# Optimization experiments

Hardware: AMD Instinct MI355X
Metric: run time of the kernel (lower is better)

## Reference

```python
import jax, jax.numpy as jnp
import numpy as np

E4M3_MAX = 448.0  # max representable value of float8_e4m3fn


def _updated_scale(amax_history, amax_now, scale):
    # roll history, insert current amax, take running max (delayed scaling)
    hist = jnp.roll(amax_history, 1).at[0].set(amax_now)
    amax = jnp.max(hist)
    sf = E4M3_MAX / amax  # scale factor (margin = 0)
    sf = jnp.where((amax > 0.0) & jnp.isfinite(amax), sf, 1.0 / scale)
    return 1.0 / sf  # dequant scale


def _qdq(x, scale, amax_history):
    # quantize-dequantize through float8_e4m3fn with dynamic amax-history scaling
    amax_now = jnp.max(jnp.abs(x)).astype(jnp.float32)
    s = _updated_scale(amax_history, amax_now, scale[0])
    q = jnp.clip(x / s, -E4M3_MAX, E4M3_MAX).astype(jnp.float8_e4m3fn)
    return q.astype(x.dtype) * s


def setup_inputs() -> dict:
    key = jax.random.key(0)
    k1, k2 = jax.random.split(key, 2)
    B, S, D, F = 4, 2048, 4096, 16384
    HL = 16  # amax_history_length
    inputs = jax.random.normal(k1, (B, S, D), jnp.float32)
    # lecun_normal: std = 1/sqrt(fan_in)
    kernel = jax.random.normal(k2, (D, F), jnp.float32) * (1.0 / np.sqrt(D))
    bias = jnp.zeros((F,), jnp.float32)
    return {
        "inputs": inputs,
        "kernel": kernel,
        "bias": bias,
        "input_scale": jnp.ones((1,), jnp.float32),
        "input_amax_history": jnp.zeros((HL,), jnp.float32),
        "kernel_scale": jnp.ones((1,), jnp.float32),
        "kernel_amax_history": jnp.zeros((HL,), jnp.float32),
        "output_grad_scale": jnp.ones((1,), jnp.float32),
        "output_grad_amax_history": jnp.zeros((HL,), jnp.float32),
    }


def reference(inputs, kernel, bias, input_scale, input_amax_history,
              kernel_scale, kernel_amax_history, output_grad_scale,
              output_grad_amax_history):
    B, S, D = inputs.shape
    x = inputs.reshape(-1, D)  # (B*S, D)
    q_x = _qdq(x, input_scale, input_amax_history)
    q_k = _qdq(kernel, kernel_scale, kernel_amax_history)
    out = q_x @ q_k  # (B*S, F)
    # bias is rounded fp32->bf16->fp32 per the module
    b = bias.astype(jnp.bfloat16).astype(jnp.float32)
    out = jax.nn.gelu(out + b)
    return out.reshape(B, S, -1)
```

## Files before the change

kernel.cpp:

```cpp
#include <hip/hip_runtime.h>
#include <hip/hip_bf16.h>

typedef __attribute__((ext_vector_type(4))) int i32x4;
typedef __attribute__((ext_vector_type(8))) int i32x8;
typedef __attribute__((ext_vector_type(16))) float f32x16;

#define E4M3_MAX 448.0f
#define AS1 __attribute__((address_space(1)))
#define AS3 __attribute__((address_space(3)))

__device__ __forceinline__ float clip448(float v) {
  return fminf(fmaxf(v, -E4M3_MAX), E4M3_MAX);
}

__device__ __forceinline__ void gld_lds16(const void* g, void* l) {
  __builtin_amdgcn_global_load_lds((const AS1 void*)g, (AS3 void*)l, 16, 0, 0);
}

__device__ __forceinline__ float gelu_f(float v) {
  float y = 0.7978845608028654f * (v + 0.044715f * v * v * v);
  float a = fabsf(y);
  float z = __expf(-2.f * a);
  float th = (1.f - z) / (1.f + z);
  th = copysignf(th, y);
  return 0.5f * v * (1.f + th);
}

__global__ void init_ws_kernel(unsigned int* amax) {
  amax[0] = 0u;
  amax[1] = 0u;
}

__global__ void amax_kernel(const float* __restrict__ x, long n4,
                            unsigned int* __restrict__ amax_out) {
  long i0 = (long)blockIdx.x * blockDim.x + threadIdx.x;
  long stride = (long)gridDim.x * blockDim.x;
  const float4* x4 = (const float4*)x;
  float m = 0.f;
  for (long i = i0; i < n4; i += stride) {
    float4 v = x4[i];
    m = fmaxf(m, fmaxf(fmaxf(fabsf(v.x), fabsf(v.y)), fmaxf(fabsf(v.z), fabsf(v.w))));
  }
#pragma unroll
  for (int off = 32; off >= 1; off >>= 1)
    m = fmaxf(m, __shfl_xor(m, off));
  __shared__ float wmax[8];
  int wid = threadIdx.x >> 6;
  if ((threadIdx.x & 63) == 0) wmax[wid] = m;
  __syncthreads();
  if (threadIdx.x == 0) {
    int nw = blockDim.x >> 6;
    float bm = wmax[0];
    for (int w = 1; w < nw; ++w) bm = fmaxf(bm, wmax[w]);
    atomicMax(amax_out, __float_as_uint(bm));
  }
}

__global__ void scale_kernel(const unsigned int* __restrict__ amax,
                             const float* __restrict__ scale_x,
                             const float* __restrict__ hist_x,
                             const float* __restrict__ scale_k,
                             const float* __restrict__ hist_k,
                             int hl, float* __restrict__ scales) {
  if (threadIdx.x != 0) return;
  float ax = __uint_as_float(amax[0]);
  for (int i = 0; i < hl - 1; ++i) ax = fmaxf(ax, hist_x[i]);
  float sfx = E4M3_MAX / ax;
  if (!(ax > 0.f && isfinite(ax))) sfx = 1.f / scale_x[0];
  float sx = 1.f / sfx;
  float ak = __uint_as_float(amax[1]);
  for (int i = 0; i < hl - 1; ++i) ak = fmaxf(ak, hist_k[i]);
  float sfk = E4M3_MAX / ak;
  if (!(ak > 0.f && isfinite(ak))) sfk = 1.f / scale_k[0];
  float sk = 1.f / sfk;
  scales[0] = sx;
  scales[1] = sk;
  scales[2] = sx * sk;
}


__global__ void quant_x_kernel(const float* __restrict__ x,
                               unsigned char* __restrict__ Aq,
                               const float* __restrict__ scales, int K) {
  const float s = scales[0];
  const int kt = blockIdx.x, mt = blockIdx.y, nkt = gridDim.x;
  __shared__ float lt[128][68];
  const int t = threadIdx.x;
  const float* src = x + (size_t)mt * 128 * K + (size_t)kt * 64;
#pragma unroll
  for (int it = 0; it < 8; ++it) {
    int row = it * 16 + (t >> 4);
    int c4 = (t & 15) * 4;
    float4 v = *(const float4*)&src[(size_t)row * K + c4];
    lt[row][c4 + 0] = v.x; lt[row][c4 + 1] = v.y;
    lt[row][c4 + 2] = v.z; lt[row][c4 + 3] = v.w;
  }
  __syncthreads();
  uint4* out = (uint4*)(Aq + ((size_t)mt * nkt + kt) * 8192);
#pragma unroll
  for (int cc = 0; cc < 2; ++cc) {
    int c = t * 2 + cc;
    int g = c >> 7, h = (c >> 6) & 1, l = c & 63;
    int row = g * 32 + (l & 31);
    int kb = (l >> 5) * 32 + h * 16;
    unsigned int w[4];
#pragma unroll
    for (int q = 0; q < 4; ++q) {
      int b = kb + q * 4;
      int p = 0;
      p = __builtin_amdgcn_cvt_pk_fp8_f32(clip448(lt[row][b+0] / s), clip448(lt[row][b+1] / s), p, false);
      p = __builtin_amdgcn_cvt_pk_fp8_f32(clip448(lt[row][b+2] / s), clip448(lt[row][b+3] / s), p, true);
      w[q] = (unsigned int)p;
    }
    out[c] = make_uint4(w[0], w[1], w[2], w[3]);
  }
}

__global__ void quant_k_kernel(const float* __restrict__ w,
                               unsigned char* __restrict__ Bq,
                               const float* __restrict__ scales, int N) {
  const float s = scales[1];
  const int kt = blockIdx.x, nt = blockIdx.y, nkt = gridDim.x;
  __shared__ float lt[64][132];
  const int t = threadIdx.x;
  const float* src = w + (size_t)kt * 64 * N + (size_t)nt * 128;
#pragma unroll
  for (int it = 0; it < 8; ++it) {
    int row = it * 8 + (t >> 5);
    int c4 = (t & 31) * 4;
    float4 v = *(const float4*)&src[(size_t)row * N + c4];
    lt[row][c4 + 0] = v.x; lt[row][c4 + 1] = v.y;
    lt[row][c4 + 2] = v.z; lt[row][c4 + 3] = v.w;
  }
  __syncthreads();
  uint4* out = (uint4*)(Bq + ((size_t)nt * nkt + kt) * 8192);
#pragma unroll
  for (int cc = 0; cc < 2; ++cc) {
    int c = t * 2 + cc;
    int g = c >> 7, h = (c >> 6) & 1, l = c & 63;
    int nl = g * 32 + (l & 31);
    int kb = (l >> 5) * 32 + h * 16;
    unsigned int w4[4];
#pragma unroll
    for (int q = 0; q < 4; ++q) {
      int b = kb + q * 4;
      int p = 0;
      p = __builtin_amdgcn_cvt_pk_fp8_f32(clip448(lt[b+0][nl] / s), clip448(lt[b+1][nl] / s), p, false);
      p = __builtin_amdgcn_cvt_pk_fp8_f32(clip448(lt[b+2][nl] / s), clip448(lt[b+3][nl] / s), p, true);
      w4[q] = (unsigned int)p;
    }
    out[c] = make_uint4(w4[0], w4[1], w4[2], w4[3]);
  }
}

#define BUFSZ 32768

#define RD_AV(dst, g_)                                                         \
  {                                                                            \
    const unsigned char* p_ =                                                  \
        lds + cb + ((g_) >> 2) * 8192 + ((g_) & 3) * 2048 + lane * 16;         \
    i32x4 lo_ = *(const i32x4*)p_;                                             \
    i32x4 hi_ = *(const i32x4*)(p_ + 1024);                                    \
    dst = __builtin_shufflevector(lo_, hi_, 0, 1, 2, 3, 4, 5, 6, 7);           \
  }
#define RD_BV(dst, g_)                                                         \
  {                                                                            \
    const unsigned char* p_ =                                                  \
        lds + cb + 16384 + ((g_) >> 2) * 8192 + ((g_) & 3) * 2048 + lane * 16; \
    i32x4 lo_ = *(const i32x4*)p_;                                             \
    i32x4 hi_ = *(const i32x4*)(p_ + 1024);                                    \
    dst = __builtin_shufflevector(lo_, hi_, 0, 1, 2, 3, 4, 5, 6, 7);           \
  }
#define MFMA1(r_, c_, a_, b_)                                                  \
  acc[r_][c_] = __builtin_amdgcn_mfma_scale_f32_32x32x64_f8f6f4(               \
      a_, b_, acc[r_][c_], 0, 0, 0, 127, 0, 127);

__global__ __launch_bounds__(512, 2) void gemm_fp8_kernel(
    const unsigned char* __restrict__ Aq, const unsigned char* __restrict__ Bq,
    const float* __restrict__ bias, const float* __restrict__ scales,
    float* __restrict__ C, int M, int N, int K) {
  __shared__ __align__(16) unsigned char lds[4 * BUFSZ];
  const float s_xk = scales[2];
  const int nkt = K >> 6;
  const int t = threadIdx.x;
  const int lane = t & 63;
  const int wid = t >> 6;
  const int wm = wid >> 2, wn = wid & 3;

  int f = blockIdx.y * gridDim.x + blockIdx.x;
  int cpx = (gridDim.x * gridDim.y) >> 3;
  int f2 = (f & 7) * cpx + (f >> 3);
  int bx = f2 % gridDim.x;
  int by = f2 / gridDim.x;

  const size_t strideT = (size_t)nkt * 8192;
  const unsigned char* gA = Aq + (size_t)(2 * by) * strideT + t * 16;
  const unsigned char* gB = Bq + (size_t)(2 * bx) * strideT + t * 16;

  f32x16 acc[4][2];
#pragma unroll
  for (int i = 0; i < 4; ++i)
#pragma unroll
    for (int j = 0; j < 2; ++j)
#pragma unroll
      for (int r = 0; r < 16; ++r) acc[i][j][r] = 0.f;

  auto stage = [&](unsigned bufbase, int kt_) {
    size_t o = (size_t)kt_ * 8192;
    unsigned char* l = lds + bufbase + wid * 1024;
    gld_lds16(gA + o,           l);
    gld_lds16(gA + strideT + o, l + 8192);
    gld_lds16(gB + o,           l + 16384);
    gld_lds16(gB + strideT + o, l + 24576);
  };

  i32x8 av0, av1, av2, av3, bv0, bv1;

  stage(0 * BUFSZ, 0);
  stage(1 * BUFSZ, 1);

  for (int kt = 0; kt < nkt; ++kt) {
    const unsigned cb = (kt & 3) * BUFSZ;

    if (kt + 2 < nkt) {
      stage(((kt + 2) & 3) * BUFSZ, kt + 2);
      asm volatile("s_waitcnt vmcnt(8)" ::: "memory");
    } else if (kt + 1 < nkt) {
      asm volatile("s_waitcnt vmcnt(4)" ::: "memory");
    } else {
      asm volatile("s_waitcnt vmcnt(0)" ::: "memory");
    }
    __builtin_amdgcn_s_barrier();
    asm volatile("" ::: "memory");

    RD_AV(av0, wm * 4 + 0);
    RD_BV(bv0, wn * 2 + 0);
    RD_BV(bv1, wn * 2 + 1);
    RD_AV(av1, wm * 4 + 1);
    RD_AV(av2, wm * 4 + 2);
    RD_AV(av3, wm * 4 + 3);

    MFMA1(0, 0, av0, bv0); MFMA1(0, 1, av0, bv1);
    MFMA1(1, 0, av1, bv0); MFMA1(1, 1, av1, bv1);
    MFMA1(2, 0, av2, bv0); MFMA1(2, 1, av2, bv1);
    MFMA1(3, 0, av3, bv0); MFMA1(3, 1, av3, bv1);
  }

  const int m0 = by * 256;
  const int n0 = bx * 256;
  float bb[2];
#pragma unroll
  for (int j = 0; j < 2; ++j) {
    int col = n0 + wn * 64 + j * 32 + (lane & 31);
    bb[j] = __bfloat162float(__float2bfloat16(bias[col]));
  }
#pragma unroll
  for (int i = 0; i < 4; ++i) {
    int rowbase = m0 + wm * 128 + i * 32 + 4 * (lane >> 5);
#pragma unroll
    for (int j = 0; j < 2; ++j) {
      int col = n0 + wn * 64 + j * 32 + (lane & 31);
#pragma unroll
      for (int r = 0; r < 16; ++r) {
        int row = rowbase + (r & 3) + 8 * (r >> 2);
        float v = acc[i][j][r] * s_xk + bb[j];
        __builtin_nontemporal_store(gelu_f(v), &C[(size_t)row * N + col]);
      }
    }
  }
}

extern "C" void kernel_launch(void* const* d_in, const int* in_sizes, int n_in,
                              void* d_out, int out_size, void* d_ws, size_t ws_size,
                              hipStream_t stream) {
  const float* inputs = (const float*)d_in[0];
  const float* kernelw = (const float*)d_in[1];
  const float* bias = (const float*)d_in[2];
  const float* input_scale = (const float*)d_in[3];
  const float* input_hist = (const float*)d_in[4];
  const float* kernel_scale = (const float*)d_in[5];
  const float* kernel_hist = (const float*)d_in[6];

  const int F = in_sizes[2];
  const int D = in_sizes[1] / F;
  const long M = (long)in_sizes[0] / D;
  const int HL = in_sizes[4];
  const int N = F, K = D;

  unsigned int* amax = (unsigned int*)d_ws;
  float* scales = (float*)((char*)d_ws + 16);
  unsigned char* Aq = (unsigned char*)d_ws + 64;
  unsigned char* Bq = Aq + (size_t)M * K;

  float* C = (float*)d_out;

  init_ws_kernel<<<1, 1, 0, stream>>>(amax);
  amax_kernel<<<2048, 256, 0, stream>>>(inputs, (long)M * K / 4, &amax[0]);
  amax_kernel<<<2048, 256, 0, stream>>>(kernelw, (long)K * N / 4, &amax[1]);
  scale_kernel<<<1, 64, 0, stream>>>(amax, input_scale, input_hist, kernel_scale,
                                     kernel_hist, HL, scales);
  quant_x_kernel<<<dim3(K / 64, M / 128), 256, 0, stream>>>(inputs, Aq, scales, K);
  quant_k_kernel<<<dim3(K / 64, N / 128), 256, 0, stream>>>(kernelw, Bq, scales, N);
  gemm_fp8_kernel<<<dim3(N / 256, M / 256), 512, 0, stream>>>(Aq, Bq, bias, scales, C,
                                                              (int)M, N, K);
}
```

Baseline: 730.6 us.

## Load B fragments directly from global into registers, stage only A in LDS

Result: slower. 811.8 us (+11.1%).

```diff
diff --git a/kernel.cpp b/kernel.cpp
--- a/kernel.cpp
+++ b/kernel.cpp
@@ -153,7 +153,7 @@
   }
 }
 
-#define BUFSZ 32768
+#define BUFSZ 16384
 
 #define RD_AV(dst, g_)                                                         \
   {                                                                            \
@@ -163,17 +163,51 @@
     i32x4 hi_ = *(const i32x4*)(p_ + 1024);                                    \
     dst = __builtin_shufflevector(lo_, hi_, 0, 1, 2, 3, 4, 5, 6, 7);           \
   }
-#define RD_BV(dst, g_)                                                         \
+
+#define LOADB(pre, kt_)                                                        \
   {                                                                            \
-    const unsigned char* p_ =                                                  \
-        lds + cb + 16384 + ((g_) >> 2) * 8192 + ((g_) & 3) * 2048 + lane * 16; \
-    i32x4 lo_ = *(const i32x4*)p_;                                             \
-    i32x4 hi_ = *(const i32x4*)(p_ + 1024);                                    \
-    dst = __builtin_shufflevector(lo_, hi_, 0, 1, 2, 3, 4, 5, 6, 7);           \
-  }
+    const i32x4* p0_ = (const i32x4*)(gB0 + (size_t)(kt_) * 8192);             \
+    const i32x4* p1_ = (const i32x4*)(gB1 + (size_t)(kt_) * 8192);             \
+    pre##0 = p0_[0];                                                           \
+    pre##1 = p0_[64];                                 \
+    pre##2 = p1_[0];                                                           \
+    pre##3 = p1_[64];                                                          \
+  }
+
 #define MFMA1(r_, c_, a_, b_)                                                  \
   acc[r_][c_] = __builtin_amdgcn_mfma_scale_f32_32x32x64_f8f6f4(               \
       a_, b_, acc[r_][c_], 0, 0, 0, 127, 0, 127);
+
+#define TILE_SEG(curpre, nxtpre, kt_)                                          \
+  {                                                                            \
+    if ((kt_) + 1 < nkt) LOADB(nxtpre, (kt_) + 1);                             \
+    if ((kt_) + 2 < nkt) stageA((((kt_) + 2) & 3) * BUFSZ, (kt_) + 2);         \
+    if ((kt_) + 2 < nkt) {                                                     \
+      asm volatile("s_waitcnt vmcnt(8)" ::: "memory");                         \
+    } else if ((kt_) + 1 < nkt) {                                              \
+      asm volatile("s_waitcnt vmcnt(6)" ::: "memory");                         \
+    } else {                                                                   \
+      asm volatile("s_waitcnt vmcnt(0)" ::: "memory");                         \
+    }                                                                          \
+    __builtin_amdgcn_sched_barrier(0);                                         \
+    __builtin_amdgcn_s_barrier();                                              \
+    {                                                                          \
+      const unsigned cb = ((kt_) & 3) * BUFSZ;                                 \
+      i32x8 av0, av1, av2, av3;                                                \
+      RD_AV(av0, wm * 4 + 0);                                                  \
+      RD_AV(av1, wm * 4 + 1);                                                  \
+      RD_AV(av2, wm * 4 + 2);                                                  \
+      RD_AV(av3, wm * 4 + 3);                                                  \
+      i32x8 bv0 =                                                              \
+          __builtin_shufflevector(curpre##0, curpre##1, 0, 1, 2, 3, 4, 5, 6, 7); \
+      i32x8 bv1 =                                                              \
+          __builtin_shufflevector(curpre##2, curpre##3, 0, 1, 2, 3, 4, 5, 6, 7); \
+      MFMA1(0, 0, av0, bv0); MFMA1(0, 1, av0, bv1);                            \
+      MFMA1(1, 0, av1, bv0); MFMA1(1, 1, av1, bv1);                            \
+      MFMA1(2, 0, av2, bv0); MFMA1(2, 1, av2, bv1);                            \
+      MFMA1(3, 0, av3, bv0); MFMA1(3, 1, av3, bv1);                            \
+    }                                                                          \
+  }
 
 __global__ __launch_bounds__(512, 2) void gemm_fp8_kernel(
     const unsigned char* __restrict__ Aq, const unsigned char* __restrict__ Bq,
@@ -195,7 +229,12 @@
 
   const size_t strideT = (size_t)nkt * 8192;
   const unsigned char* gA = Aq + (size_t)(2 * by) * strideT + t * 16;
-  const unsigned char* gB = Bq + (size_t)(2 * bx) * strideT + t * 16;
+
+  const int g0 = wn * 2 + 0, g1 = wn * 2 + 1;
+  const unsigned char* gB0 =
+      Bq + (size_t)(2 * bx + (g0 >> 2)) * strideT + (g0 & 3) * 2048 + lane * 16;
+  const unsigned char* gB1 =
+      Bq + (size_t)(2 * bx + (g1 >> 2)) * strideT + (g1 & 3) * 2048 + lane * 16;
 
   f32x16 acc[4][2];
 #pragma unroll
@@ -205,45 +244,26 @@
 #pragma unroll
       for (int r = 0; r < 16; ++r) acc[i][j][r] = 0.f;
 
-  auto stage = [&](unsigned bufbase, int kt_) {
+  auto stageA = [&](unsigned bufbase, int kt_) {
     size_t o = (size_t)kt_ * 8192;
     unsigned char* l = lds + bufbase + wid * 1024;
     gld_lds16(gA + o,           l);
     gld_lds16(gA + strideT + o, l + 8192);
-    gld_lds16(gB + o,           l + 16384);
-    gld_lds16(gB + strideT + o, l + 24576);
   };
 
-  i32x8 av0, av1, av2, av3, bv0, bv1;
-
-  stage(0 * BUFSZ, 0);
-  stage(1 * BUFSZ, 1);
-
-  for (int kt = 0; kt < nkt; ++kt) {
-    const unsigned cb = (kt & 3) * BUFSZ;
-
-    if (kt + 2 < nkt) {
-      stage(((kt + 2) & 3) * BUFSZ, kt + 2);
-      asm volatile("s_waitcnt vmcnt(8)" ::: "memory");
-    } else if (kt + 1 < nkt) {
-      asm volatile("s_waitcnt vmcnt(4)" ::: "memory");
-    } else {
-      asm volatile("s_waitcnt vmcnt(0)" ::: "memory");
-    }
-    __builtin_amdgcn_s_barrier();
-    asm volatile("" ::: "memory");
-
-    RD_AV(av0, wm * 4 + 0);
-    RD_BV(bv0, wn * 2 + 0);
-    RD_BV(bv1, wn * 2 + 1);
-    RD_AV(av1, wm * 4 + 1);
-    RD_AV(av2, wm * 4 + 2);
-    RD_AV(av3, wm * 4 + 3);
-
-    MFMA1(0, 0, av0, bv0); MFMA1(0, 1, av0, bv1);
-    MFMA1(1, 0, av1, bv0); MFMA1(1, 1, av1, bv1);
-    MFMA1(2, 0, av2, bv0); MFMA1(2, 1, av2, bv1);
-    MFMA1(3, 0, av3, bv0); MFMA1(3, 1, av3, bv1);
+  i32x4 bAr0, bAr1, bAr2, bAr3;
+  i32x4 bBr0, bBr1, bBr2, bBr3;
+
+  stageA(0 * BUFSZ, 0);
+  stageA(1 * BUFSZ, 1);
+  LOADB(bAr, 0);
+  asm volatile("s_waitcnt vmcnt(0)" ::: "memory");
+  __builtin_amdgcn_sched_barrier(0);
+  __builtin_amdgcn_s_barrier();
+
+  for (int kt = 0; kt < nkt; kt += 2) {
+    TILE_SEG(bAr, bBr, kt);
+    TILE_SEG(bBr, bAr, kt + 1);
   }
 
   const int m0 = by * 256;
```

## Double-buffer LDS fragment registers to overlap reads with MFMA

Applied to the files above, without the earlier changes.

Result: slower. 1.386 ms (+89.7%).

```diff
diff --git a/kernel.cpp b/kernel.cpp
--- a/kernel.cpp
+++ b/kernel.cpp
@@ -155,25 +155,36 @@
 
 #define BUFSZ 32768
 
-#define RD_AV(dst, g_)                                                         \
+#define RD8(dst, byteoff)                                                      \
   {                                                                            \
-    const unsigned char* p_ =                                                  \
-        lds + cb + ((g_) >> 2) * 8192 + ((g_) & 3) * 2048 + lane * 16;         \
+    const unsigned char* p_ = lds + (byteoff) + lane * 16;                     \
     i32x4 lo_ = *(const i32x4*)p_;                                             \
     i32x4 hi_ = *(const i32x4*)(p_ + 1024);                                    \
     dst = __builtin_shufflevector(lo_, hi_, 0, 1, 2, 3, 4, 5, 6, 7);           \
   }
-#define RD_BV(dst, g_)                                                         \
+
+#define READ_FRAGS(pre, bufbase)                                               \
   {                                                                            \
-    const unsigned char* p_ =                                                  \
-        lds + cb + 16384 + ((g_) >> 2) * 8192 + ((g_) & 3) * 2048 + lane * 16; \
-    i32x4 lo_ = *(const i32x4*)p_;                                             \
-    i32x4 hi_ = *(const i32x4*)(p_ + 1024);                                    \
-    dst = __builtin_shufflevector(lo_, hi_, 0, 1, 2, 3, 4, 5, 6, 7);           \
-  }
+    const unsigned cb_ = (bufbase);                                            \
+    RD8(pre##a0, cb_ + ag0);                                                   \
+    RD8(pre##a1, cb_ + ag1);                                                   \
+    RD8(pre##a2, cb_ + ag2);                                                   \
+    RD8(pre##a3, cb_ + ag3);                                                   \
+    RD8(pre##b0, cb_ + bg0);                                                   \
+    RD8(pre##b1, cb_ + bg1);                                                   \
+  }
+
 #define MFMA1(r_, c_, a_, b_)                                                  \
   acc[r_][c_] = __builtin_amdgcn_mfma_scale_f32_32x32x64_f8f6f4(               \
       a_, b_, acc[r_][c_], 0, 0, 0, 127, 0, 127);
+
+#define MFMA_ALL(pre)                                                          \
+  {                                                                            \
+    MFMA1(0, 0, pre##a0, pre##b0); MFMA1(0, 1, pre##a0, pre##b1);              \
+    MFMA1(1, 0, pre##a1, pre##b0); MFMA1(1, 1, pre##a1, pre##b1);              \
+    MFMA1(2, 0, pre##a2, pre##b0); MFMA1(2, 1, pre##a2, pre##b1);              \
+    MFMA1(3, 0, pre##a3, pre##b0); MFMA1(3, 1, pre##a3, pre##b1);              \
+  }
 
 __global__ __launch_bounds__(512, 2) void gemm_fp8_kernel(
     const unsigned char* __restrict__ Aq, const unsigned char* __restrict__ Bq,
@@ -187,6 +198,15 @@
   const int wid = t >> 6;
   const int wm = wid >> 2, wn = wid & 3;
 
+  const int gA0 = wm * 4;
+  const unsigned ag0 = ((gA0 + 0) >> 2) * 8192 + ((gA0 + 0) & 3) * 2048;
+  const unsigned ag1 = ((gA0 + 1) >> 2) * 8192 + ((gA0 + 1) & 3) * 2048;
+  const unsigned ag2 = ((gA0 + 2) >> 2) * 8192 + ((gA0 + 2) & 3) * 2048;
+  const unsigned ag3 = ((gA0 + 3) >> 2) * 8192 + ((gA0 + 3) & 3) * 2048;
+  const int gB0 = wn * 2;
+  const unsigned bg0 = 16384 + ((gB0 + 0) >> 2) * 8192 + ((gB0 + 0) & 3) * 2048;
+  const unsigned bg1 = 16384 + ((gB0 + 1) >> 2) * 8192 + ((gB0 + 1) & 3) * 2048;
+
   int f = blockIdx.y * gridDim.x + blockIdx.x;
   int cpx = (gridDim.x * gridDim.y) >> 3;
   int f2 = (f & 7) * cpx + (f >> 3);
@@ -214,36 +234,35 @@
     gld_lds16(gB + strideT + o, l + 24576);
   };
 
-  i32x8 av0, av1, av2, av3, bv0, bv1;
+  i32x8 f0a0, f0a1, f0a2, f0a3, f0b0, f0b1;
+  i32x8 f1a0, f1a1, f1a2, f1a3, f1b0, f1b1;
 
   stage(0 * BUFSZ, 0);
   stage(1 * BUFSZ, 1);
-
-  for (int kt = 0; kt < nkt; ++kt) {
-    const unsigned cb = (kt & 3) * BUFSZ;
-
+  asm volatile("s_waitcnt vmcnt(4)" ::: "memory");
+  __builtin_amdgcn_s_barrier();
+  READ_FRAGS(f0, 0);
+
+  for (int kt = 0; kt < nkt; kt += 2) {
     if (kt + 2 < nkt) {
       stage(((kt + 2) & 3) * BUFSZ, kt + 2);
-      asm volatile("s_waitcnt vmcnt(8)" ::: "memory");
-    } else if (kt + 1 < nkt) {
       asm volatile("s_waitcnt vmcnt(4)" ::: "memory");
     } else {
       asm volatile("s_waitcnt vmcnt(0)" ::: "memory");
     }
     __builtin_amdgcn_s_barrier();
-    asm volatile("" ::: "memory");
-
-    RD_AV(av0, wm * 4 + 0);
-    RD_BV(bv0, wn * 2 + 0);
-    RD_BV(bv1, wn * 2 + 1);
-    RD_AV(av1, wm * 4 + 1);
-    RD_AV(av2, wm * 4 + 2);
-    RD_AV(av3, wm * 4 + 3);
-
-    MFMA1(0, 0, av0, bv0); MFMA1(0, 1, av0, bv1);
-    MFMA1(1, 0, av1, bv0); MFMA1(1, 1, av1, bv1);
-    MFMA1(2, 0, av2, bv0); MFMA1(2, 1, av2, bv1);
-    MFMA1(3, 0, av3, bv0); MFMA1(3, 1, av3, bv1);
+    if (kt + 1 < nkt) READ_FRAGS(f1, ((kt + 1) & 3) * BUFSZ);
+    MFMA_ALL(f0);
+
+    if (kt + 3 < nkt) {
+      stage(((kt + 3) & 3) * BUFSZ, kt + 3);
+      asm volatile("s_waitcnt vmcnt(4)" ::: "memory");
+    } else {
+      asm volatile("s_waitcnt vmcnt(0)" ::: "memory");
+    }
+    __builtin_amdgcn_s_barrier();
+    if (kt + 2 < nkt) READ_FRAGS(f0, ((kt + 2) & 3) * BUFSZ);
+    MFMA_ALL(f1);
   }
 
   const int m0 = by * 256;
```

## Process K tiles in pairs with one barrier-synchronized refill per pair

Applied to the files above, without the earlier changes.

Measured after the change: 753.2 us. 1.03x slower.

```diff
diff --git a/kernel.cpp b/kernel.cpp
--- a/kernel.cpp
+++ b/kernel.cpp
@@ -155,25 +155,33 @@
 
 #define BUFSZ 32768
 
-#define RD_AV(dst, g_)                                                         \
+#define RD8(dst, byteoff)                                                      \
   {                                                                            \
-    const unsigned char* p_ =                                                  \
-        lds + cb + ((g_) >> 2) * 8192 + ((g_) & 3) * 2048 + lane * 16;         \
+    const unsigned char* p_ = lds + (byteoff) + lane * 16;                     \
     i32x4 lo_ = *(const i32x4*)p_;                                             \
     i32x4 hi_ = *(const i32x4*)(p_ + 1024);                                    \
     dst = __builtin_shufflevector(lo_, hi_, 0, 1, 2, 3, 4, 5, 6, 7);           \
   }
-#define RD_BV(dst, g_)                                                         \
-  {                                                                            \
-    const unsigned char* p_ =                                                  \
-        lds + cb + 16384 + ((g_) >> 2) * 8192 + ((g_) & 3) * 2048 + lane * 16; \
-    i32x4 lo_ = *(const i32x4*)p_;                                             \
-    i32x4 hi_ = *(const i32x4*)(p_ + 1024);                                    \
-    dst = __builtin_shufflevector(lo_, hi_, 0, 1, 2, 3, 4, 5, 6, 7);           \
-  }
+
 #define MFMA1(r_, c_, a_, b_)                                                  \
   acc[r_][c_] = __builtin_amdgcn_mfma_scale_f32_32x32x64_f8f6f4(               \
       a_, b_, acc[r_][c_], 0, 0, 0, 127, 0, 127);
+
+#define TILE_BLOCK(tile_)                                                      \
+  {                                                                            \
+    const unsigned cb = ((tile_) & 3) * BUFSZ;                                 \
+    i32x8 av0, av1, av2, av3, bv0, bv1;                                        \
+    RD8(av0, cb + ag0);                                                        \
+    RD8(bv0, cb + bg0);                                                        \
+    RD8(bv1, cb + bg1);                                                        \
+    RD8(av1, cb + ag1);                                                        \
+    RD8(av2, cb + ag2);                                                        \
+    RD8(av3, cb + ag3);                                                        \
+    MFMA1(0, 0, av0, bv0); MFMA1(0, 1, av0, bv1);                              \
+    MFMA1(1, 0, av1, bv0); MFMA1(1, 1, av1, bv1);                              \
+    MFMA1(2, 0, av2, bv0); MFMA1(2, 1, av2, bv1);                              \
+    MFMA1(3, 0, av3, bv0); MFMA1(3, 1, av3, bv1);                              \
+  }
 
 __global__ __launch_bounds__(512, 2) void gemm_fp8_kernel(
     const unsigned char* __restrict__ Aq, const unsigned char* __restrict__ Bq,
@@ -182,10 +190,20 @@
   __shared__ __align__(16) unsigned char lds[4 * BUFSZ];
   const float s_xk = scales[2];
   const int nkt = K >> 6;
+  const int npair = nkt >> 1;
   const int t = threadIdx.x;
   const int lane = t & 63;
   const int wid = t >> 6;
   const int wm = wid >> 2, wn = wid & 3;
+
+  const int gA0 = wm * 4;
+  const unsigned ag0 = ((gA0 + 0) >> 2) * 8192 + ((gA0 + 0) & 3) * 2048;
+  const unsigned ag1 = ((gA0 + 1) >> 2) * 8192 + ((gA0 + 1) & 3) * 2048;
+  const unsigned ag2 = ((gA0 + 2) >> 2) * 8192 + ((gA0 + 2) & 3) * 2048;
+  const unsigned ag3 = ((gA0 + 3) >> 2) * 8192 + ((gA0 + 3) & 3) * 2048;
+  const int gB0g = wn * 2;
+  const unsigned bg0 = 16384 + ((gB0g + 0) >> 2) * 8192 + ((gB0g + 0) & 3) * 2048;
+  const unsigned bg1 = 16384 + ((gB0g + 1) >> 2) * 8192 + ((gB0g + 1) & 3) * 2048;
 
   int f = blockIdx.y * gridDim.x + blockIdx.x;
   int cpx = (gridDim.x * gridDim.y) >> 3;
@@ -205,45 +223,36 @@
 #pragma unroll
       for (int r = 0; r < 16; ++r) acc[i][j][r] = 0.f;
 
-  auto stage = [&](unsigned bufbase, int kt_) {
+  auto stage = [&](int kt_) {
     size_t o = (size_t)kt_ * 8192;
-    unsigned char* l = lds + bufbase + wid * 1024;
+    unsigned char* l = lds + (kt_ & 3) * BUFSZ + wid * 1024;
     gld_lds16(gA + o,           l);
     gld_lds16(gA + strideT + o, l + 8192);
     gld_lds16(gB + o,           l + 16384);
     gld_lds16(gB + strideT + o, l + 24576);
   };
 
-  i32x8 av0, av1, av2, av3, bv0, bv1;
-
-  stage(0 * BUFSZ, 0);
-  stage(1 * BUFSZ, 1);
-
-  for (int kt = 0; kt < nkt; ++kt) {
-    const unsigned cb = (kt & 3) * BUFSZ;
-
-    if (kt + 2 < nkt) {
-      stage(((kt + 2) & 3) * BUFSZ, kt + 2);
+  stage(0); stage(1); stage(2); stage(3);
+
+  for (int p = 0; p < npair; ++p) {
+    const int u = 2 * p, v = 2 * p + 1;
+
+    if (p + 1 < npair) {
       asm volatile("s_waitcnt vmcnt(8)" ::: "memory");
-    } else if (kt + 1 < nkt) {
-      asm volatile("s_waitcnt vmcnt(4)" ::: "memory");
     } else {
       asm volatile("s_waitcnt vmcnt(0)" ::: "memory");
     }
     __builtin_amdgcn_s_barrier();
     asm volatile("" ::: "memory");
 
-    RD_AV(av0, wm * 4 + 0);
-    RD_BV(bv0, wn * 2 + 0);
-    RD_BV(bv1, wn * 2 + 1);
-    RD_AV(av1, wm * 4 + 1);
-    RD_AV(av2, wm * 4 + 2);
-    RD_AV(av3, wm * 4 + 3);
-
-    MFMA1(0, 0, av0, bv0); MFMA1(0, 1, av0, bv1);
-    MFMA1(1, 0, av1, bv0); MFMA1(1, 1, av1, bv1);
-    MFMA1(2, 0, av2, bv0); MFMA1(2, 1, av2, bv1);
-    MFMA1(3, 0, av3, bv0); MFMA1(3, 1, av3, bv1);
+    TILE_BLOCK(u);
+    TILE_BLOCK(v);
+
+    __builtin_amdgcn_s_barrier();
+    if (p + 2 < npair) {
+      stage(u + 4);
+      stage(v + 4);
+    }
   }
 
   const int m0 = by * 256;
```
